# Optimization experiments

Hardware: AMD Instinct MI355X
Metric: run time of the kernel (lower is better)

The kernel has to match this reference:

```python
import jax, jax.numpy as jnp
import numpy as np

B, H, W, C = 16, 384, 512, 3

def setup_inputs() -> dict:
    key = jax.random.key(0)
    k1, k2, k3 = jax.random.split(key, 3)
    source_img = jax.random.normal(k1, (B, H, W, C), jnp.float32)
    depth_map = jax.random.uniform(k2, (B, H, W), jnp.float32, minval=0.1, maxval=10.0)
    pose = jax.random.normal(k3, (B, 6), jnp.float32)
    intrinsics = jnp.array([[500.0, 0.0, W / 2.0],
                            [0.0, 500.0, H / 2.0],
                            [0.0, 0.0, 1.0]], jnp.float32)
    return {"source_img": source_img, "depth_map": depth_map, "pose": pose,
            "intrinsics": intrinsics}


def _pose_vec2mat(pose):
    # ProjectionLayer scales: translation *= 0.01, rotation (euler rx,ry,rz) *= 0.001
    t = pose[:, :3] * 0.01                       # [B,3]
    r = pose[:, 3:] * 0.001                      # [B,3] euler angles (rx, ry, rz)
    cx, cy, cz = jnp.cos(r[:, 0]), jnp.cos(r[:, 1]), jnp.cos(r[:, 2])
    sx, sy, sz = jnp.sin(r[:, 0]), jnp.sin(r[:, 1]), jnp.sin(r[:, 2])
    z = jnp.zeros_like(cx); o = jnp.ones_like(cx)
    Rz = jnp.stack([cz, -sz, z, sz, cz, z, z, z, o], -1).reshape(-1, 3, 3)
    Ry = jnp.stack([cy, z, sy, z, o, z, -sy, z, cy], -1).reshape(-1, 3, 3)
    Rx = jnp.stack([o, z, z, z, cx, -sx, z, sx, cx], -1).reshape(-1, 3, 3)
    R = Rz @ Ry @ Rx                             # [B,3,3]
    top = jnp.concatenate([R, t[:, :, None]], -1)            # [B,3,4]
    bottom = jnp.broadcast_to(jnp.array([[[0., 0., 0., 1.]]], top.dtype),
                              (top.shape[0], 1, 4))
    return jnp.concatenate([top, bottom], 1)     # [B,4,4]


def _bilinear_sample(img, x, y):
    # img: [B,H,W,C]; x,y: [B,HW] pixel coords. Border-clamped bilinear gather.
    Bn, Hn, Wn, Cn = img.shape
    x0f = jnp.floor(x); y0f = jnp.floor(y)
    x1f = x0f + 1.0;    y1f = y0f + 1.0
    wa = (x1f - x) * (y1f - y)
    wb = (x1f - x) * (y - y0f)
    wc = (x - x0f) * (y1f - y)
    wd = (x - x0f) * (y - y0f)
    x0 = jnp.clip(x0f, 0, Wn - 1).astype(jnp.int32)
    x1 = jnp.clip(x1f, 0, Wn - 1).astype(jnp.int32)
    y0 = jnp.clip(y0f, 0, Hn - 1).astype(jnp.int32)
    y1 = jnp.clip(y1f, 0, Hn - 1).astype(jnp.int32)
    flat = img.reshape(Bn, Hn * Wn, Cn)
    def gather(yi, xi):
        idx = (yi * Wn + xi)[..., None]                      # [B,HW,1]
        return jnp.take_along_axis(flat, idx, axis=1)        # [B,HW,C]
    out = (wa[..., None] * gather(y0, x0) + wb[..., None] * gather(y1, x0)
           + wc[..., None] * gather(y0, x1) + wd[..., None] * gather(y1, x1))
    return out.reshape(Bn, Hn, Wn, Cn)


def reference(source_img, depth_map, pose, intrinsics):
    Bn, Hn, Wn, Cn = source_img.shape
    dt = source_img.dtype
    T = _pose_vec2mat(pose)                                  # [B,4,4] target->source
    Kinv = jnp.linalg.inv(intrinsics)                        # [3,3]
    xs, ys = jnp.meshgrid(jnp.arange(Wn, dtype=dt), jnp.arange(Hn, dtype=dt))
    pix = jnp.stack([xs, ys, jnp.ones_like(xs)], 0).reshape(3, Hn * Wn)  # [3,HW]
    # pixel2cam: depth * K^-1 @ [u,v,1]
    cam = (Kinv @ pix)[None] * depth_map.reshape(Bn, 1, Hn * Wn)         # [B,3,HW]
    cam_h = jnp.concatenate([cam, jnp.ones((Bn, 1, Hn * Wn), dt)], 1)    # [B,4,HW]
    K4 = jnp.zeros((4, 4), dt).at[:3, :3].set(intrinsics).at[3, 3].set(1.0)
    proj = K4[None] @ T                                      # [B,4,4]
    p = proj @ cam_h                                         # [B,4,HW]
    x_src = p[:, 0] / (p[:, 2] + 1e-10)
    y_src = p[:, 1] / (p[:, 2] + 1e-10)
    return _bilinear_sample(source_img, x_src, y_src)        # [B,H,W,C]
```

## Files before the change

### kernel.cpp

```cpp
#include <hip/hip_runtime.h>
#include <math.h>

#define Bn  16
#define Hn  384
#define Wn  512
#define HWn (Hn * Wn)

__global__ __launch_bounds__(256) void ProjectionLayer_678604833211_kernel(
    const float* __restrict__ src,
    const float* __restrict__ depth,
    const float* __restrict__ pose,
    const float* __restrict__ intr,
    float* __restrict__ out)
{
    __shared__ float S[16];
    const int b = blockIdx.y;

    if (threadIdx.x == 0) {
        const float fx = intr[0], cx = intr[2], fy = intr[4], cy = intr[5];
        const float tx = pose[b * 6 + 0] * 0.01f;
        const float ty = pose[b * 6 + 1] * 0.01f;
        const float tz = pose[b * 6 + 2] * 0.01f;
        const float rx = pose[b * 6 + 3] * 0.001f;
        const float ry = pose[b * 6 + 4] * 0.001f;
        const float rz = pose[b * 6 + 5] * 0.001f;
        const float cX = cosf(rx), sX = sinf(rx);
        const float cY = cosf(ry), sY = sinf(ry);
        const float cZ = cosf(rz), sZ = sinf(rz);
        const float R00 = cZ * cY;
        const float R01 = -sZ * cX + cZ * sY * sX;
        const float R02 =  sZ * sX + cZ * sY * cX;
        const float R10 = sZ * cY;
        const float R11 =  cZ * cX + sZ * sY * sX;
        const float R12 = -cZ * sX + sZ * sY * cX;
        const float R20 = -sY;
        const float R21 = cY * sX;
        const float R22 = cY * cX;
        S[0]  = fx * R00 + cx * R20;
        S[1]  = fx * R01 + cx * R21;
        S[2]  = fx * R02 + cx * R22;
        S[3]  = fx * tx  + cx * tz;
        S[4]  = fy * R10 + cy * R20;
        S[5]  = fy * R11 + cy * R21;
        S[6]  = fy * R12 + cy * R22;
        S[7]  = fy * ty  + cy * tz;
        S[8]  = R20;
        S[9]  = R21;
        S[10] = R22;
        S[11] = tz;
        S[12] = 1.0f / fx;
        S[13] = -cx / fx;
        S[14] = 1.0f / fy;
        S[15] = -cy / fy;
    }
    __syncthreads();

    const int tid = blockIdx.x * blockDim.x + threadIdx.x;
    if (tid >= HWn) return;
    const int u = tid & (Wn - 1);
    const int v = tid >> 9;

    const float d = depth[(size_t)b * HWn + tid];

    const float camx = fmaf((float)u, S[12], S[13]) * d;
    const float camy = fmaf((float)v, S[14], S[15]) * d;

    const float p0 = fmaf(S[0], camx, fmaf(S[1], camy, fmaf(S[2],  d, S[3])));
    const float p1 = fmaf(S[4], camx, fmaf(S[5], camy, fmaf(S[6],  d, S[7])));
    const float p2 = fmaf(S[8], camx, fmaf(S[9], camy, fmaf(S[10], d, S[11])));

    const float inv = 1.0f / (p2 + 1e-10f);
    const float x = p0 * inv;
    const float y = p1 * inv;

    const float x0f = floorf(x), y0f = floorf(y);
    const float ax = x - x0f;
    const float ay = y - y0f;
    const float bx = (x0f + 1.0f) - x;
    const float by = (y0f + 1.0f) - y;
    const float wa = bx * by;
    const float wb = bx * ay;
    const float wc = ax * by;
    const float wd = ax * ay;

    const int x0 = (int)fminf(fmaxf(x0f,        0.0f), (float)(Wn - 1));
    const int x1 = (int)fminf(fmaxf(x0f + 1.0f, 0.0f), (float)(Wn - 1));
    const int y0 = (int)fminf(fmaxf(y0f,        0.0f), (float)(Hn - 1));
    const int y1 = (int)fminf(fmaxf(y0f + 1.0f, 0.0f), (float)(Hn - 1));

    const float* base = src + (size_t)b * HWn * 3;
    const float* pa = base + (size_t)(y0 * Wn + x0) * 3;
    const float* pb = base + (size_t)(y1 * Wn + x0) * 3;
    const float* pc = base + (size_t)(y0 * Wn + x1) * 3;
    const float* pd = base + (size_t)(y1 * Wn + x1) * 3;

    const float o0 = wa * pa[0] + wb * pb[0] + wc * pc[0] + wd * pd[0];
    const float o1 = wa * pa[1] + wb * pb[1] + wc * pc[1] + wd * pd[1];
    const float o2 = wa * pa[2] + wb * pb[2] + wc * pc[2] + wd * pd[2];

    float* q = out + ((size_t)b * HWn + tid) * 3;
    q[0] = o0;
    q[1] = o1;
    q[2] = o2;
}

extern "C" void kernel_launch(void* const* d_in, const int* in_sizes, int n_in,
                              void* d_out, int out_size, void* d_ws, size_t ws_size,
                              hipStream_t stream) {
    const float* src   = (const float*)d_in[0];
    const float* depth = (const float*)d_in[1];
    const float* pose  = (const float*)d_in[2];
    const float* intr  = (const float*)d_in[3];
    float* out = (float*)d_out;

    dim3 grid(HWn / 256, Bn);
    dim3 block(256);
    ProjectionLayer_678604833211_kernel<<<grid, block, 0, stream>>>(
        src, depth, pose, intr, out);
}
```

Before: 111.8 us.

## Process four pixels per thread with vectorized nontemporal loads and stores

Each thread now handles four consecutive pixels. It loads depth as a float4 and writes the twelve output floats as three float4 nontemporal stores, replacing strided scalar stores. Horizontally adjacent bilinear taps are fetched as one 24-byte contiguous read per row, with a fallback path when clamping collapses them. The grid shrinks by a factor of four, which lowers parallelism and raises per-thread register pressure in exchange for wider memory transactions.

```diff
diff --git a/kernel.cpp b/kernel.cpp
--- a/kernel.cpp
+++ b/kernel.cpp
@@ -5,6 +5,8 @@
 #define Hn  384
 #define Wn  512
 #define HWn (Hn * Wn)
+
+typedef float f4 __attribute__((ext_vector_type(4)));
 
 __global__ __launch_bounds__(256) void ProjectionLayer_678604833211_kernel(
     const float* __restrict__ src,
@@ -55,53 +57,83 @@
     }
     __syncthreads();
 
-    const int tid = blockIdx.x * blockDim.x + threadIdx.x;
-    if (tid >= HWn) return;
-    const int u = tid & (Wn - 1);
-    const int v = tid >> 9;
+    const int tid0 = (blockIdx.x * 256 + threadIdx.x) * 4;
+    const int u0 = tid0 & (Wn - 1);
+    const int v  = tid0 >> 9;
 
-    const float d = depth[(size_t)b * HWn + tid];
+    const f4 dvec = __builtin_nontemporal_load(
+        (const f4*)(depth + (size_t)b * HWn + tid0));
 
-    const float camx = fmaf((float)u, S[12], S[13]) * d;
-    const float camy = fmaf((float)v, S[14], S[15]) * d;
+    const float m0 = S[0],  m1 = S[1],  m2 = S[2],  m3 = S[3];
+    const float m4 = S[4],  m5 = S[5],  m6 = S[6],  m7 = S[7];
+    const float m8 = S[8],  m9 = S[9],  m10 = S[10], m11 = S[11];
+    const float ifx = S[12], nfx = S[13], ify = S[14], nfy = S[15];
 
-    const float p0 = fmaf(S[0], camx, fmaf(S[1], camy, fmaf(S[2],  d, S[3])));
-    const float p1 = fmaf(S[4], camx, fmaf(S[5], camy, fmaf(S[6],  d, S[7])));
-    const float p2 = fmaf(S[8], camx, fmaf(S[9], camy, fmaf(S[10], d, S[11])));
+    const float camy_unit = fmaf((float)v, ify, nfy);
+    const float* base = src + (size_t)b * HWn * 3;
 
-    const float inv = 1.0f / (p2 + 1e-10f);
-    const float x = p0 * inv;
-    const float y = p1 * inv;
+    float o[12];
 
-    const float x0f = floorf(x), y0f = floorf(y);
-    const float ax = x - x0f;
-    const float ay = y - y0f;
-    const float bx = (x0f + 1.0f) - x;
-    const float by = (y0f + 1.0f) - y;
-    const float wa = bx * by;
-    const float wb = bx * ay;
-    const float wc = ax * by;
-    const float wd = ax * ay;
+    #pragma unroll
+    for (int j = 0; j < 4; ++j) {
+        const float d = dvec[j];
+        const float camx = fmaf((float)(u0 + j), ifx, nfx) * d;
+        const float camy = camy_unit * d;
 
-    const int x0 = (int)fminf(fmaxf(x0f,        0.0f), (float)(Wn - 1));
-    const int x1 = (int)fminf(fmaxf(x0f + 1.0f, 0.0f), (float)(Wn - 1));
-    const int y0 = (int)fminf(fmaxf(y0f,        0.0f), (float)(Hn - 1));
-    const int y1 = (int)fminf(fmaxf(y0f + 1.0f, 0.0f), (float)(Hn - 1));
+        const float p0 = fmaf(m0, camx, fmaf(m1, camy, fmaf(m2,  d, m3)));
+        const float p1 = fmaf(m4, camx, fmaf(m5, camy, fmaf(m6,  d, m7)));
+        const float p2 = fmaf(m8, camx, fmaf(m9, camy, fmaf(m10, d, m11)));
 
-    const float* base = src + (size_t)b * HWn * 3;
-    const float* pa = base + (size_t)(y0 * Wn + x0) * 3;
-    const float* pb = base + (size_t)(y1 * Wn + x0) * 3;
-    const float* pc = base + (size_t)(y0 * Wn + x1) * 3;
-    const float* pd = base + (size_t)(y1 * Wn + x1) * 3;
+        const float inv = 1.0f / (p2 + 1e-10f);
+        const float x = p0 * inv;
+        const float y = p1 * inv;
 
-    const float o0 = wa * pa[0] + wb * pb[0] + wc * pc[0] + wd * pd[0];
-    const float o1 = wa * pa[1] + wb * pb[1] + wc * pc[1] + wd * pd[1];
-    const float o2 = wa * pa[2] + wb * pb[2] + wc * pc[2] + wd * pd[2];
+        const float x0f = floorf(x), y0f = floorf(y);
+        const float ax = x - x0f;
+        const float ay = y - y0f;
+        const float bx = (x0f + 1.0f) - x;
+        const float by = (y0f + 1.0f) - y;
+        const float wa = bx * by;
+        const float wb = bx * ay;
+        const float wc = ax * by;
+        const float wd = ax * ay;
 
-    float* q = out + ((size_t)b * HWn + tid) * 3;
-    q[0] = o0;
-    q[1] = o1;
-    q[2] = o2;
+        const int x0 = (int)fminf(fmaxf(x0f,        0.0f), (float)(Wn - 1));
+        const int x1 = (int)fminf(fmaxf(x0f + 1.0f, 0.0f), (float)(Wn - 1));
+        const int y0 = (int)fminf(fmaxf(y0f,        0.0f), (float)(Hn - 1));
+        const int y1 = (int)fminf(fmaxf(y0f + 1.0f, 0.0f), (float)(Hn - 1));
+
+        const float* r0 = base + (size_t)(y0 * Wn + x0) * 3;
+        const float* r1 = base + (size_t)(y1 * Wn + x0) * 3;
+
+        float A0, A1, A2, C0, C1, C2, B0, B1, B2, D0, D1, D2;
+        if (x1 == x0 + 1) {
+            float t0[6], t1[6];
+            __builtin_memcpy(t0, r0, 24);
+            __builtin_memcpy(t1, r1, 24);
+            A0 = t0[0]; A1 = t0[1]; A2 = t0[2];
+            C0 = t0[3]; C1 = t0[4]; C2 = t0[5];
+            B0 = t1[0]; B1 = t1[1]; B2 = t1[2];
+            D0 = t1[3]; D1 = t1[4]; D2 = t1[5];
+        } else {
+            A0 = r0[0]; A1 = r0[1]; A2 = r0[2];
+            C0 = A0; C1 = A1; C2 = A2;
+            B0 = r1[0]; B1 = r1[1]; B2 = r1[2];
+            D0 = B0; D1 = B1; D2 = B2;
+        }
+
+        o[j * 3 + 0] = wa * A0 + wb * B0 + wc * C0 + wd * D0;
+        o[j * 3 + 1] = wa * A1 + wb * B1 + wc * C1 + wd * D1;
+        o[j * 3 + 2] = wa * A2 + wb * B2 + wc * C2 + wd * D2;
+    }
+
+    f4* q = (f4*)(out + ((size_t)b * HWn + tid0) * 3);
+    f4 s0 = {o[0], o[1], o[2],  o[3]};
+    f4 s1 = {o[4], o[5], o[6],  o[7]};
+    f4 s2 = {o[8], o[9], o[10], o[11]};
+    __builtin_nontemporal_store(s0, q + 0);
+    __builtin_nontemporal_store(s1, q + 1);
+    __builtin_nontemporal_store(s2, q + 2);
 }
 
 extern "C" void kernel_launch(void* const* d_in, const int* in_sizes, int n_in,
@@ -113,7 +145,7 @@
     const float* intr  = (const float*)d_in[3];
     float* out = (float*)d_out;
 
-    dim3 grid(HWn / 256, Bn);
+    dim3 grid(HWn / (256 * 4), Bn);
     dim3 block(256);
     ProjectionLayer_678604833211_kernel<<<grid, block, 0, stream>>>(
         src, depth, pose, intr, out);
```

New measurement: 127.7 us. 1.14x slower.

## Process 8 pixels per thread with vector loads, paired-texel gathers and XCD-aware block mapping

Applied to the files above, without the earlier changes.

Each thread now handles 8 consecutive pixels of a row. Depth is read with two nontemporal float4 loads, and the output is written with six nontemporal float4 stores. The bilinear gather now does two 24-byte reads of adjacent texel pairs instead of four 12-byte reads, with weights adjusted so clamped borders stay correct. Blocks are remapped so each XCD works on a contiguous band of rows within one batch, which should improve L2 locality for the gathers. The cost is fewer threads (12288 blocks become 1536) and more registers per thread, which may limit latency hiding.

```diff
diff --git a/kernel.cpp b/kernel.cpp
--- a/kernel.cpp
+++ b/kernel.cpp
@@ -5,6 +5,8 @@
 #define Hn  384
 #define Wn  512
 #define HWn (Hn * Wn)
+
+typedef float f4 __attribute__((ext_vector_type(4)));
 
 __global__ __launch_bounds__(256) void ProjectionLayer_678604833211_kernel(
     const float* __restrict__ src,
@@ -14,7 +16,13 @@
     float* __restrict__ out)
 {
     __shared__ float S[16];
-    const int b = blockIdx.y;
+
+    const int n    = blockIdx.x;
+    const int xcd  = n & 7;
+    const int m    = n >> 3;
+    const int b    = m / 12;
+    const int sub  = m - b * 12;
+    const int rowblk = xcd * 12 + sub;
 
     if (threadIdx.x == 0) {
         const float fx = intr[0], cx = intr[2], fy = intr[4], cy = intr[5];
@@ -55,53 +63,77 @@
     }
     __syncthreads();
 
-    const int tid = blockIdx.x * blockDim.x + threadIdx.x;
-    if (tid >= HWn) return;
-    const int u = tid & (Wn - 1);
-    const int v = tid >> 9;
+    const int wave = threadIdx.x >> 6;
+    const int lane = threadIdx.x & 63;
+    const int row  = rowblk * 4 + wave;
+    const int u0   = lane * 8;
 
-    const float d = depth[(size_t)b * HWn + tid];
+    const float m0 = S[0],  m1 = S[1],  m2  = S[2],  m3  = S[3];
+    const float m4 = S[4],  m5 = S[5],  m6  = S[6],  m7  = S[7];
+    const float m8 = S[8],  m9 = S[9],  m10 = S[10], m11 = S[11];
+    const float ifx = S[12], nfx = S[13], ify = S[14], nfy = S[15];
 
-    const float camx = fmaf((float)u, S[12], S[13]) * d;
-    const float camy = fmaf((float)v, S[14], S[15]) * d;
+    const size_t px0 = (size_t)b * HWn + (size_t)row * Wn + u0;
+    const f4 dA = __builtin_nontemporal_load((const f4*)(depth + px0));
+    const f4 dB = __builtin_nontemporal_load((const f4*)(depth + px0 + 4));
+    const float dv[8] = {dA.x, dA.y, dA.z, dA.w, dB.x, dB.y, dB.z, dB.w};
 
-    const float p0 = fmaf(S[0], camx, fmaf(S[1], camy, fmaf(S[2],  d, S[3])));
-    const float p1 = fmaf(S[4], camx, fmaf(S[5], camy, fmaf(S[6],  d, S[7])));
-    const float p2 = fmaf(S[8], camx, fmaf(S[9], camy, fmaf(S[10], d, S[11])));
+    const float camy_u = fmaf((float)row, ify, nfy);
+    const float* __restrict__ base = src + (size_t)b * HWn * 3;
 
-    const float inv = 1.0f / (p2 + 1e-10f);
-    const float x = p0 * inv;
-    const float y = p1 * inv;
+    float o[24];
 
-    const float x0f = floorf(x), y0f = floorf(y);
-    const float ax = x - x0f;
-    const float ay = y - y0f;
-    const float bx = (x0f + 1.0f) - x;
-    const float by = (y0f + 1.0f) - y;
-    const float wa = bx * by;
-    const float wb = bx * ay;
-    const float wc = ax * by;
-    const float wd = ax * ay;
+    #pragma unroll
+    for (int j = 0; j < 8; ++j) {
+        const float d = dv[j];
+        const float camx = fmaf((float)(u0 + j), ifx, nfx) * d;
+        const float camy = camy_u * d;
 
-    const int x0 = (int)fminf(fmaxf(x0f,        0.0f), (float)(Wn - 1));
-    const int x1 = (int)fminf(fmaxf(x0f + 1.0f, 0.0f), (float)(Wn - 1));
-    const int y0 = (int)fminf(fmaxf(y0f,        0.0f), (float)(Hn - 1));
-    const int y1 = (int)fminf(fmaxf(y0f + 1.0f, 0.0f), (float)(Hn - 1));
+        const float p0 = fmaf(m0, camx, fmaf(m1, camy, fmaf(m2,  d, m3)));
+        const float p1 = fmaf(m4, camx, fmaf(m5, camy, fmaf(m6,  d, m7)));
+        const float p2 = fmaf(m8, camx, fmaf(m9, camy, fmaf(m10, d, m11)));
 
-    const float* base = src + (size_t)b * HWn * 3;
-    const float* pa = base + (size_t)(y0 * Wn + x0) * 3;
-    const float* pb = base + (size_t)(y1 * Wn + x0) * 3;
-    const float* pc = base + (size_t)(y0 * Wn + x1) * 3;
-    const float* pd = base + (size_t)(y1 * Wn + x1) * 3;
+        const float inv = 1.0f / (p2 + 1e-10f);
+        const float x = p0 * inv;
+        const float y = p1 * inv;
 
-    const float o0 = wa * pa[0] + wb * pb[0] + wc * pc[0] + wd * pd[0];
-    const float o1 = wa * pa[1] + wb * pb[1] + wc * pc[1] + wd * pd[1];
-    const float o2 = wa * pa[2] + wb * pb[2] + wc * pc[2] + wd * pd[2];
+        const float x0f = floorf(x), y0f = floorf(y);
+        const float ax = x - x0f;
+        const float ay = y - y0f;
+        const float bx = (x0f + 1.0f) - x;
+        const float by = (y0f + 1.0f) - y;
 
-    float* q = out + ((size_t)b * HWn + tid) * 3;
-    q[0] = o0;
-    q[1] = o1;
-    q[2] = o2;
+        const int x0 = (int)fminf(fmaxf(x0f,        0.0f), 511.0f);
+        const int x1 = (int)fminf(fmaxf(x0f + 1.0f, 0.0f), 511.0f);
+        const int p  = (int)fminf(fmaxf(x0f,        0.0f), 510.0f);
+        const int y0 = (int)fminf(fmaxf(y0f,        0.0f), 383.0f);
+        const int y1 = (int)fminf(fmaxf(y0f + 1.0f, 0.0f), 383.0f);
+
+        const bool loA = (x0 == p);
+        const bool hiC = (x1 == p + 1);
+        const float xl = (loA ? bx : 0.0f) + (hiC ? 0.0f : ax);
+        const float xh = (loA ? 0.0f : bx) + (hiC ? ax : 0.0f);
+
+        const float* r0 = base + (size_t)(y0 * Wn + p) * 3;
+        const float* r1 = base + (size_t)(y1 * Wn + p) * 3;
+        float t0[6], t1[6];
+        __builtin_memcpy(t0, r0, 24);
+        __builtin_memcpy(t1, r1, 24);
+
+        o[j * 3 + 0] = fmaf(by, fmaf(xl, t0[0], xh * t0[3]),
+                            ay * fmaf(xl, t1[0], xh * t1[3]));
+        o[j * 3 + 1] = fmaf(by, fmaf(xl, t0[1], xh * t0[4]),
+                            ay * fmaf(xl, t1[1], xh * t1[4]));
+        o[j * 3 + 2] = fmaf(by, fmaf(xl, t0[2], xh * t0[5]),
+                            ay * fmaf(xl, t1[2], xh * t1[5]));
+    }
+
+    f4* q = (f4*)(out + px0 * 3);
+    #pragma unroll
+    for (int k = 0; k < 6; ++k) {
+        f4 s = {o[4 * k + 0], o[4 * k + 1], o[4 * k + 2], o[4 * k + 3]};
+        __builtin_nontemporal_store(s, q + k);
+    }
 }
 
 extern "C" void kernel_launch(void* const* d_in, const int* in_sizes, int n_in,
@@ -113,7 +145,7 @@
     const float* intr  = (const float*)d_in[3];
     float* out = (float*)d_out;
 
-    dim3 grid(HWn / 256, Bn);
+    dim3 grid(Bn * 96);
     dim3 block(256);
     ProjectionLayer_678604833211_kernel<<<grid, block, 0, stream>>>(
         src, depth, pose, intr, out);
```

Result: slower. 162.1 us (+45.0%).
